# Kernel optimization log

Hardware: AMD Instinct MI355X
Metric: run time of the kernel (lower is better)

Reference implementation:

```python
import jax, jax.numpy as jnp
import numpy as np

N, E, B, H, L = 50000, 500000, 64, 64, 4


def setup_inputs() -> dict:
    key = jax.random.key(0)
    ks = jax.random.split(key, 32)
    def w(k, shp, fan_in):
        s = 1.0 / np.sqrt(fan_in)
        return jax.random.uniform(k, shp, jnp.float32, -s, s)
    inp = {
        "v0": jax.random.normal(ks[0], (N, 1), jnp.float32),
        "v1": jax.random.normal(ks[1], (N, 1), jnp.float32),
        "dist": jax.random.uniform(ks[2], (E, 1), jnp.float32),
        "edge_index": jax.random.randint(ks[3], (2, E), 0, N, jnp.int32),
        "batch": jnp.sort(jax.random.randint(ks[4], (N,), 0, B, jnp.int32)),
        "batch_size": B,
        # embeddings / per-input linears
        "wte": jax.random.normal(ks[5], (2, H), jnp.float32),
        "W_in0": w(ks[6], (H, 1), 1), "b_in0": w(ks[7], (H,), 1),
        "W_in1": w(ks[8], (H, 1), 1), "b_in1": w(ks[9], (H,), 1),
        "W_out0": w(ks[10], (1, H), H), "b_out0": w(ks[11], (1,), H),
        "W_out1": w(ks[12], (1, H), H), "b_out1": w(ks[13], (1,), H),
        "W_edge": w(ks[14], (H, 1), 1), "b_edge": w(ks[15], (H,), 1),
        # shared GraphBlock (ModuleList([block]*L) shares weights)
        "W_el": w(ks[16], (H, 2 * H), 2 * H), "b_el": w(ks[17], (H,), 2 * H),
        "W_n1": w(ks[18], (4 * H, 3 * H), 3 * H), "b_n1": w(ks[19], (4 * H,), 3 * H),
        "W_n2": w(ks[20], (H, 4 * H), 4 * H), "b_n2": w(ks[21], (H,), 4 * H),
        "W_gl": w(ks[22], (H, 2 * H), 2 * H), "b_gl": w(ks[23], (H,), 2 * H),
        # shared LSTMCell
        "W_ih": w(ks[24], (4 * H, H), H), "W_hh": w(ks[25], (4 * H, H), H),
        "b_ih": w(ks[26], (4 * H,), H), "b_hh": w(ks[27], (4 * H,), H),
    }
    return inp


def _forward(v0, v1, dist, edge_index, batch, batch_size,
             wte, W_in0, b_in0, W_in1, b_in1, W_out0, b_out0, W_out1, b_out1,
             W_edge, b_edge, W_el, b_el, W_n1, b_n1, W_n2, b_n2, W_gl, b_gl,
             W_ih, W_hh, b_ih, b_hh):
    # x = sum_i (type_embedding_i + Linear_i(v_i))  -> [N, H]
    x = (wte[0] + v0 @ W_in0.T + b_in0) + (wte[1] + v1 @ W_in1.T + b_in1)
    e = dist @ W_edge.T + b_edge                      # [E, H]
    u = jnp.zeros((batch_size, x.shape[-1]), x.dtype)  # [B, H]
    row, col = edge_index[0], edge_index[1]
    n_nodes = x.shape[0]
    cs = []
    for _ in range(L):  # shared weights across layers (faithful to [block]*L)
        # edge MLP on gathered source features, scatter-max to destination nodes
        msg = jax.nn.relu(jnp.concatenate([x[row], e], axis=-1) @ W_el.T + b_el)
        agg = jax.ops.segment_max(msg, col, num_segments=n_nodes)
        agg = jnp.where(jnp.isfinite(agg), agg, 0.0)  # empty segments -> 0
        # node MLP with residual
        h1 = jax.nn.relu(jnp.concatenate([agg, x, u[batch]], axis=-1) @ W_n1.T + b_n1)
        x = x + h1 @ W_n2.T + b_n2
        # global update: per-graph max over nodes
        x_u = jax.ops.segment_max(x, batch, num_segments=batch_size)
        x_u = jnp.where(jnp.isfinite(x_u), x_u, 0.0)
        u = u + jax.nn.relu(jnp.concatenate([x_u, u], axis=-1) @ W_gl.T + b_gl)
        # LSTMCell with zero initial (h, c) every layer (hidden_states=None path)
        gates = u @ W_ih.T + b_ih + b_hh  # h_prev = 0 so W_hh term vanishes
        i_g, f_g, g_g, o_g = jnp.split(gates, 4, axis=-1)
        c = jax.nn.sigmoid(i_g) * jnp.tanh(g_g)        # c_prev = 0
        u = jax.nn.sigmoid(o_g) * jnp.tanh(c)
        cs.append(c)
    outs = jnp.stack([x @ W_out0.T + b_out0, x @ W_out1.T + b_out1])  # [2, N, 1]
    return outs, jnp.stack(cs)  # ([2,N,1], [L,B,H])


def reference(v0, v1, dist, edge_index, batch, batch_size,
              wte, W_in0, b_in0, W_in1, b_in1, W_out0, b_out0, W_out1, b_out1,
              W_edge, b_edge, W_el, b_el, W_n1, b_n1, W_n2, b_n2, W_gl, b_gl,
              W_ih, W_hh, b_ih, b_hh):
    return _forward(v0, v1, dist, edge_index, batch, batch_size,
                    wte, W_in0, b_in0, W_in1, b_in1, W_out0, b_out0, W_out1, b_out1,
                    W_edge, b_edge, W_el, b_el, W_n1, b_n1, W_n2, b_n2, W_gl, b_gl,
                    W_ih, W_hh, b_ih, b_hh)
```

## Files before the change

### kernel.cpp

```cpp
#include <hip/hip_runtime.h>


typedef __attribute__((ext_vector_type(8))) short short8;
typedef __attribute__((ext_vector_type(4))) float f32x4;

__device__ __forceinline__ unsigned short f2bf(float f) {
  union { float f; unsigned u; } v; v.f = f;
  unsigned r = v.u + 0x7FFFu + ((v.u >> 16) & 1u);
  return (unsigned short)(r >> 16);
}
__device__ __forceinline__ float bf2f(unsigned short s) {
  return __uint_as_float((unsigned)s << 16);
}
__device__ __forceinline__ unsigned enc_ordered(float f) {
  unsigned u = __float_as_uint(f);
  return (u >> 31) ? ~u : (u | 0x80000000u);
}

__global__ void k_init(const float* __restrict__ v0, const float* __restrict__ v1,
                       const float* __restrict__ wte,
                       const float* __restrict__ Wi0, const float* __restrict__ bi0,
                       const float* __restrict__ Wi1, const float* __restrict__ bi1,
                       const int* __restrict__ batch,
                       int* __restrict__ gstart, int* __restrict__ gend,
                       float* __restrict__ x,
                       float* __restrict__ u, unsigned* __restrict__ xu_enc,
                       unsigned short* __restrict__ W1b, unsigned short* __restrict__ W2b,
                       unsigned short* __restrict__ Welb,
                       const float* __restrict__ W_n1, const float* __restrict__ W_n2,
                       const float* __restrict__ W_el,
                       const float* __restrict__ b_el,
                       const float* __restrict__ W_edge, const float* __restrict__ b_edge,
                       float* __restrict__ p, float* __restrict__ q,
                       float* __restrict__ c0, float* __restrict__ c1,
                       float* __restrict__ c2,
                       int* __restrict__ deg, int* __restrict__ cur, int N) {
  int gt = blockIdx.x * 256 + threadIdx.x;
  int NH = N * 64;
  if (gt < NH) {
    int n = gt >> 6, h = gt & 63;
    x[gt] = wte[h] + wte[64 + h] + bi0[h] + bi1[h] + v0[n] * Wi0[h] + v1[n] * Wi1[h];
    if (h == 0) {
      int bg = batch[n];
      if (n == 0 || batch[n - 1] != bg) gstart[bg] = n;
      if (n == N - 1 || batch[n + 1] != bg) gend[bg] = n + 1;
    }
    return;
  }
  int i = gt - NH;
  if (i < 4096) {
    u[i] = 0.f;
  } else if (i < 8192) {
    xu_enc[i - 4096] = 0x007FFFFFu;
  } else if (i < 8192 + 49152) {
    int j = i - 8192;
    W1b[j] = f2bf(W_n1[j]);
  } else if (i < 8192 + 49152 + 16384) {
    int j = i - 57344;
    W2b[j] = f2bf(W_n2[j]);
  } else if (i < 77824) {
    int j = i - 73728;
    Welb[j] = f2bf(W_el[(j >> 6) * 128 + (j & 63)]);
  } else if (i < 77824 + N) {
    deg[i - 77824] = 0;
  } else if (i < 77824 + 2 * N) {
    cur[i - 77824 - N] = 0;
  } else if (i < 77824 + 2 * N + 64) {
    int h = i - 77824 - 2 * N;
    float pp = 0.f, qq = 0.f, s0 = 0.f, s1 = 0.f, s2 = 0.f;
    for (int k = 0; k < 64; ++k) {
      float w2 = W_el[h * 128 + 64 + k];
      pp += w2 * W_edge[k];
      qq += w2 * b_edge[k];
      float w1 = W_el[h * 128 + k];
      float base = wte[k] + wte[64 + k] + bi0[k] + bi1[k];
      s0 += w1 * base;
      s1 += w1 * Wi0[k];
      s2 += w1 * Wi1[k];
    }
    p[h] = pp; q[h] = qq + b_el[h];
    c0[h] = s0; c1[h] = s1; c2[h] = s2;
  }
}

__global__ __launch_bounds__(256) void k_hist(const int* __restrict__ eidx,
                                              int* __restrict__ deg, int E) {
  int e = blockIdx.x * 256 + threadIdx.x;
  if (e < E) atomicAdd(&deg[eidx[E + e]], 1);
}

__global__ __launch_bounds__(256) void k_scan1(const int* __restrict__ deg,
                                               int* __restrict__ off,
                                               int* __restrict__ bsum, int N) {
  __shared__ int s[256];
  int b = blockIdx.x, t = threadIdx.x;
  int i0 = b * 512 + t * 2;
  int v0 = (i0 < N) ? deg[i0] : 0;
  int v1 = (i0 + 1 < N) ? deg[i0 + 1] : 0;
  int sum = v0 + v1;
  s[t] = sum;
  __syncthreads();
  for (int d = 1; d < 256; d <<= 1) {
    int val = (t >= d) ? s[t - d] : 0;
    __syncthreads();
    s[t] += val;
    __syncthreads();
  }
  int excl = s[t] - sum;
  if (i0 < N) off[i0] = excl + v0;
  if (i0 + 1 < N) off[i0 + 1] = excl + v0 + v1;
  if (t == 255) bsum[b] = s[t];
}

__global__ void k_scan2(int* __restrict__ bsum, int nb) {
  __shared__ int s[128];
  int t = threadIdx.x;
  int v = (t < nb) ? bsum[t] : 0;
  s[t] = v;
  __syncthreads();
  for (int d = 1; d < 128; d <<= 1) {
    int val = (t >= d) ? s[t - d] : 0;
    __syncthreads();
    s[t] += val;
    __syncthreads();
  }
  if (t < nb) bsum[t] = s[t] - v;
}

__global__ __launch_bounds__(256) void k_scatter(const int* __restrict__ eidx,
                                                 const float* __restrict__ dist,
                                                 const int* __restrict__ off,
                                                 const int* __restrict__ bsum,
                                                 int* __restrict__ cur,
                                                 uint2* __restrict__ spack, int E) {
  int e = blockIdx.x * 256 + threadIdx.x;
  if (e >= E) return;
  int c = eidx[E + e];
  int base = (c == 0) ? 0 : (off[c - 1] + bsum[(c - 1) >> 9]);
  int pos = base + atomicAdd(&cur[c], 1);
  spack[pos] = make_uint2((unsigned)eidx[e] | ((unsigned)(c & 31) << 27),
                          __float_as_uint(dist[e]));
}

template <int MODE>
__global__ __launch_bounds__(256) void k_node(
    const int* __restrict__ off, const int* __restrict__ bsum,
    const uint2* __restrict__ spack,
    const float* __restrict__ p, const float* __restrict__ q,
    const float* __restrict__ c0, const float* __restrict__ c1,
    const float* __restrict__ c2,
    const float* __restrict__ v0, const float* __restrict__ v1,
    float* __restrict__ x, unsigned short* __restrict__ y_bf,
    const int* __restrict__ batch, const float* __restrict__ u,
    const unsigned short* __restrict__ W1b, const unsigned short* __restrict__ W2b,
    const unsigned short* __restrict__ Welb,
    const float* __restrict__ b_n1, const float* __restrict__ b_n2,
    unsigned* __restrict__ xu_enc,
    float* __restrict__ bmaxA, float* __restrict__ bmaxB,
    int* __restrict__ bgidA, int* __restrict__ bgidB,
    const float* __restrict__ Wo0, const float* __restrict__ bo0,
    const float* __restrict__ Wo1, const float* __restrict__ bo1,
    float* __restrict__ outp, int N) {
  __shared__ __align__(16) char inb[32 * 384];
  __shared__ __align__(16) char h1T[32 * 512];
  __shared__ uint2 smeta[256];
  __shared__ int sgb[32];
  int t = threadIdx.x;
  int n0 = blockIdx.x * 32;
  int lane = t & 63, wv = t >> 6;
  int lr = lane & 15;
  int lk8 = (lane >> 4) << 3;
  int jo = (lane >> 4) << 2;
  int swzr = (lr & 7) << 4;
  int h0 = wv * 16 + jo;

  float4 xo[2];
#pragma unroll
  for (int nt = 0; nt < 2; ++nt) {
    int node = n0 + nt * 16 + lr;
    xo[nt] = (node < N) ? *(const float4*)(x + (size_t)node * 64 + h0)
                        : make_float4(0.f, 0.f, 0.f, 0.f);
  }
  int nd_s = t >> 3, ko = t & 7;
  int node_s = n0 + nd_s;
  float4 ua = make_float4(0.f, 0.f, 0.f, 0.f), ub = ua;
  if (node_s < N) {
    int g = batch[node_s];
    const float4* u4 = (const float4*)u;
    ua = u4[g * 16 + ko * 2];
    ub = u4[g * 16 + ko * 2 + 1];
  }
  if (t < 32) sgb[t] = batch[min(n0 + t, N - 1)];

  int* aggi = (int*)h1T;
#pragma unroll
  for (int i = 0; i < 8; ++i) aggi[t + i * 256] = 0;

#pragma unroll
  for (int nt = 0; nt < 2; ++nt) {
    int nd = nt * 16 + lr;
    unsigned lo = (unsigned)f2bf(xo[nt].x) | ((unsigned)f2bf(xo[nt].y) << 16);
    unsigned hi = (unsigned)f2bf(xo[nt].z) | ((unsigned)f2bf(xo[nt].w) << 16);
    *(uint2*)(inb + nd * 384 + ((128 + h0 * 2) ^ ((nd & 7) << 4))) = make_uint2(lo, hi);
  }
  {
    int swz = (nd_s & 7) << 4;
    uint4 uv;
    uv.x = f2bf(ua.x) | ((unsigned)f2bf(ua.y) << 16);
    uv.y = f2bf(ua.z) | ((unsigned)f2bf(ua.w) << 16);
    uv.z = f2bf(ub.x) | ((unsigned)f2bf(ub.y) << 16);
    uv.w = f2bf(ub.z) | ((unsigned)f2bf(ub.w) << 16);
    *(uint4*)(inb + nd_s * 384 + ((256 + ko * 16) ^ swz)) = uv;
  }
  __syncthreads();

  {
    int last = min(n0 + 31, N - 1);
    int ebase = (n0 == 0) ? 0 : (off[n0 - 1] + bsum[(n0 - 1) >> 9]);
    int eend = off[last] + bsum[last >> 9];
    int total = eend - ebase;
    int q4 = total >> 2;
    int wb = ebase + wv * q4;
    int we = (wv == 3) ? eend : (wb + q4);
    uint2* sm = smeta + wv * 64;
    int half = lane >> 5, l31 = lane & 31;
    const unsigned* y32 = (const unsigned*)y_bf + l31;
    float2 p2 = *(const float2*)(p + 2 * l31);
    float2 q2 = *(const float2*)(q + 2 * l31);
    float2 c02 = make_float2(0.f, 0.f), c12 = c02, c22 = c02;
    if (MODE == 0) {
      c02 = *(const float2*)(c0 + 2 * l31);
      c12 = *(const float2*)(c1 + 2 * l31);
      c22 = *(const float2*)(c2 + 2 * l31);
    }
    float m0 = 0.f, m1 = 0.f;
    int ccur = -1;
    uint2 r = make_uint2(0u, 0u);
    if (wb < we) {
      int cnt = min(64, we - wb);
      if (lane < cnt) r = spack[wb + lane];
    }
    for (int cb = wb; cb < we; cb += 64) {
      int ccnt = min(64, we - cb);
      sm[lane] = r;
      int nb = cb + 64;
      if (nb < we) {
        int ncnt = we - nb;
        if (lane < ncnt) r = spack[nb + lane];
      }
      int nfull = ccnt >> 1;
      int i = 0;
      for (; i + 8 <= nfull; i += 8) {
        uint2 e[8]; unsigned yd[8]; float va[8], vb[8];
#pragma unroll
        for (int k = 0; k < 8; ++k) e[k] = sm[2 * (i + k) + half];
#pragma unroll
        for (int k = 0; k < 8; ++k) {
          unsigned row = e[k].x & 0x07FFFFFFu;
          if (MODE == 0) { va[k] = v0[row]; vb[k] = v1[row]; }
          else yd[k] = y32[row << 5];
        }
#pragma unroll
        for (int k = 0; k < 8; ++k) {
          float y0f, y1f;
          if (MODE == 0) {
            y0f = fmaf(vb[k], c22.x, fmaf(va[k], c12.x, c02.x));
            y1f = fmaf(vb[k], c22.y, fmaf(va[k], c12.y, c02.y));
          } else {
            y0f = __uint_as_float(yd[k] << 16);
            y1f = __uint_as_float(yd[k] & 0xFFFF0000u);
          }
          float d = __uint_as_float(e[k].y);
          float g0 = fmaxf(fmaf(d, p2.x, y0f + q2.x), 0.f);
          float g1 = fmaxf(fmaf(d, p2.y, y1f + q2.y), 0.f);
          int c = (int)(e[k].x >> 27);
          if (c != ccur) {
            if (ccur >= 0) {
              atomicMax(&aggi[ccur * 64 + 2 * l31], __float_as_int(m0));
              atomicMax(&aggi[ccur * 64 + 2 * l31 + 1], __float_as_int(m1));
            }
            ccur = c; m0 = g0; m1 = g1;
          } else { m0 = fmaxf(m0, g0); m1 = fmaxf(m1, g1); }
        }
      }
      for (; 2 * i < ccnt; ++i) {
        int idx = 2 * i + half;
        bool val = idx < ccnt;
        uint2 e = sm[val ? idx : 0];
        unsigned row = e.x & 0x07FFFFFFu;
        float y0f, y1f;
        if (MODE == 0) {
          float a = v0[row], b = v1[row];
          y0f = fmaf(b, c22.x, fmaf(a, c12.x, c02.x));
          y1f = fmaf(b, c22.y, fmaf(a, c12.y, c02.y));
        } else {
          unsigned yd = y32[row << 5];
          y0f = __uint_as_float(yd << 16);
          y1f = __uint_as_float(yd & 0xFFFF0000u);
        }
        float d = __uint_as_float(e.y);
        float g0 = val ? fmaxf(fmaf(d, p2.x, y0f + q2.x), 0.f) : 0.f;
        float g1 = val ? fmaxf(fmaf(d, p2.y, y1f + q2.y), 0.f) : 0.f;
        int c = val ? (int)(e.x >> 27) : ccur;
        if (c != ccur) {
          if (ccur >= 0) {
            atomicMax(&aggi[ccur * 64 + 2 * l31], __float_as_int(m0));
            atomicMax(&aggi[ccur * 64 + 2 * l31 + 1], __float_as_int(m1));
          }
          ccur = c; m0 = g0; m1 = g1;
        } else { m0 = fmaxf(m0, g0); m1 = fmaxf(m1, g1); }
      }
    }
    if (ccur >= 0) {
      atomicMax(&aggi[ccur * 64 + 2 * l31], __float_as_int(m0));
      atomicMax(&aggi[ccur * 64 + 2 * l31 + 1], __float_as_int(m1));
    }
  }
  __syncthreads();

  {
    int swz = (nd_s & 7) << 4;
    const float4* ag4 = (const float4*)(h1T);
    float4 aa = ag4[nd_s * 16 + ko * 2];
    float4 ab = ag4[nd_s * 16 + ko * 2 + 1];
    uint4 av;
    av.x = f2bf(aa.x) | ((unsigned)f2bf(aa.y) << 16);
    av.y = f2bf(aa.z) | ((unsigned)f2bf(aa.w) << 16);
    av.z = f2bf(ab.x) | ((unsigned)f2bf(ab.y) << 16);
    av.w = f2bf(ab.z) | ((unsigned)f2bf(ab.w) << 16);
    *(uint4*)(inb + nd_s * 384 + ((ko * 16) ^ swz)) = av;
  }
  __syncthreads();

  int w = wv;

  f32x4 acc[4][2];
#pragma unroll
  for (int ot = 0; ot < 4; ++ot)
#pragma unroll
    for (int nt = 0; nt < 2; ++nt) acc[ot][nt] = (f32x4){0.f, 0.f, 0.f, 0.f};
  const unsigned short* W1p = W1b + (w * 64 + lr) * 192 + lk8;
#pragma unroll
  for (int ks = 0; ks < 6; ++ks) {
    int kb = ks * 64 + lk8 * 2;
    short8 b0 = *(const short8*)(inb + lr * 384 + (kb ^ swzr));
    short8 b1 = *(const short8*)(inb + (16 + lr) * 384 + (kb ^ swzr));
#pragma unroll
    for (int ot = 0; ot < 4; ++ot) {
      short8 a = *(const short8*)(W1p + ot * (16 * 192) + ks * 32);
      acc[ot][0] = __builtin_amdgcn_mfma_f32_16x16x32_bf16(a, b0, acc[ot][0], 0, 0, 0);
      acc[ot][1] = __builtin_amdgcn_mfma_f32_16x16x32_bf16(a, b1, acc[ot][1], 0, 0, 0);
    }
  }
  __syncthreads();
#pragma unroll
  for (int ot = 0; ot < 4; ++ot) {
    int o = w * 64 + ot * 16 + jo;
    float4 bs = *(const float4*)(b_n1 + o);
#pragma unroll
    for (int nt = 0; nt < 2; ++nt) {
      int nd = nt * 16 + lr;
      unsigned lo = (unsigned)f2bf(fmaxf(acc[ot][nt][0] + bs.x, 0.f)) |
                    ((unsigned)f2bf(fmaxf(acc[ot][nt][1] + bs.y, 0.f)) << 16);
      unsigned hi = (unsigned)f2bf(fmaxf(acc[ot][nt][2] + bs.z, 0.f)) |
                    ((unsigned)f2bf(fmaxf(acc[ot][nt][3] + bs.w, 0.f)) << 16);
      *(uint2*)(h1T + nd * 512 + ((o * 2) ^ ((nd & 7) << 4))) = make_uint2(lo, hi);
    }
  }
  __syncthreads();

  f32x4 acc2[2] = {{0.f, 0.f, 0.f, 0.f}, {0.f, 0.f, 0.f, 0.f}};
  const unsigned short* W2p = W2b + (w * 16 + lr) * 256 + lk8;
#pragma unroll
  for (int ks = 0; ks < 8; ++ks) {
    short8 a = *(const short8*)(W2p + ks * 32);
    int kb = ks * 64 + lk8 * 2;
    short8 b0 = *(const short8*)(h1T + lr * 512 + (kb ^ swzr));
    short8 b1 = *(const short8*)(h1T + (16 + lr) * 512 + (kb ^ swzr));
    acc2[0] = __builtin_amdgcn_mfma_f32_16x16x32_bf16(a, b0, acc2[0], 0, 0, 0);
    acc2[1] = __builtin_amdgcn_mfma_f32_16x16x32_bf16(a, b1, acc2[1], 0, 0, 0);
  }
  float4 b2 = *(const float4*)(b_n2 + h0);
  char* xnb = inb;
  float4 xn[2];
#pragma unroll
  for (int nt = 0; nt < 2; ++nt) {
    int nd = nt * 16 + lr;
    int node = n0 + nd;
    xn[nt].x = xo[nt].x + acc2[nt][0] + b2.x;
    xn[nt].y = xo[nt].y + acc2[nt][1] + b2.y;
    xn[nt].z = xo[nt].z + acc2[nt][2] + b2.z;
    xn[nt].w = xo[nt].w + acc2[nt][3] + b2.w;
    if (node >= N) xn[nt] = make_float4(0.f, 0.f, 0.f, 0.f);
    if (MODE != 2 && node < N) *(float4*)(x + (size_t)node * 64 + h0) = xn[nt];
    if (MODE != 2) {
      unsigned lo = (unsigned)f2bf(xn[nt].x) | ((unsigned)f2bf(xn[nt].y) << 16);
      unsigned hi = (unsigned)f2bf(xn[nt].z) | ((unsigned)f2bf(xn[nt].w) << 16);
      *(uint2*)(xnb + nd * 128 + ((h0 * 2) ^ ((nd & 7) << 4))) = make_uint2(lo, hi);
    }
  }

  {
    const float NEG = -__builtin_huge_valf();
    int gA = sgb[0], gB = sgb[31];
    float a0 = NEG, a1 = NEG, a2 = NEG, a3 = NEG;
    float e0 = NEG, e1 = NEG, e2 = NEG, e3 = NEG;
#pragma unroll
    for (int nt = 0; nt < 2; ++nt) {
      int nd = nt * 16 + lr;
      if (n0 + nd < N) {
        int g = sgb[nd];
        if (g == gA) {
          a0 = fmaxf(a0, xn[nt].x); a1 = fmaxf(a1, xn[nt].y);
          a2 = fmaxf(a2, xn[nt].z); a3 = fmaxf(a3, xn[nt].w);
        } else if (g == gB) {
          e0 = fmaxf(e0, xn[nt].x); e1 = fmaxf(e1, xn[nt].y);
          e2 = fmaxf(e2, xn[nt].z); e3 = fmaxf(e3, xn[nt].w);
        } else {
          unsigned* xe = xu_enc + g * 64 + h0;
          atomicMax(xe + 0, enc_ordered(xn[nt].x));
          atomicMax(xe + 1, enc_ordered(xn[nt].y));
          atomicMax(xe + 2, enc_ordered(xn[nt].z));
          atomicMax(xe + 3, enc_ordered(xn[nt].w));
        }
      }
    }
#pragma unroll
    for (int msk = 1; msk <= 8; msk <<= 1) {
      a0 = fmaxf(a0, __shfl_xor(a0, msk)); a1 = fmaxf(a1, __shfl_xor(a1, msk));
      a2 = fmaxf(a2, __shfl_xor(a2, msk)); a3 = fmaxf(a3, __shfl_xor(a3, msk));
      e0 = fmaxf(e0, __shfl_xor(e0, msk)); e1 = fmaxf(e1, __shfl_xor(e1, msk));
      e2 = fmaxf(e2, __shfl_xor(e2, msk)); e3 = fmaxf(e3, __shfl_xor(e3, msk));
    }
    if (lr == 0) {
      size_t base = (size_t)blockIdx.x * 64 + h0;
      bmaxA[base + 0] = a0; bmaxA[base + 1] = a1;
      bmaxA[base + 2] = a2; bmaxA[base + 3] = a3;
      bmaxB[base + 0] = e0; bmaxB[base + 1] = e1;
      bmaxB[base + 2] = e2; bmaxB[base + 3] = e3;
    }
    if (t == 0) {
      bgidA[blockIdx.x] = gA;
      bgidB[blockIdx.x] = (gB == gA) ? -1 : gB;
    }
  }
  __syncthreads();

  if (MODE != 2) {
    f32x4 acc3[2] = {{0.f, 0.f, 0.f, 0.f}, {0.f, 0.f, 0.f, 0.f}};
    const unsigned short* W3p = Welb + (w * 16 + lr) * 64 + lk8;
#pragma unroll
    for (int ks = 0; ks < 2; ++ks) {
      short8 a = *(const short8*)(W3p + ks * 32);
      int kb = ks * 64 + lk8 * 2;
      short8 b0 = *(const short8*)(xnb + lr * 128 + (kb ^ swzr));
      short8 b1 = *(const short8*)(xnb + (16 + lr) * 128 + (kb ^ swzr));
      acc3[0] = __builtin_amdgcn_mfma_f32_16x16x32_bf16(a, b0, acc3[0], 0, 0, 0);
      acc3[1] = __builtin_amdgcn_mfma_f32_16x16x32_bf16(a, b1, acc3[1], 0, 0, 0);
    }
    int o0 = w * 16 + jo;
#pragma unroll
    for (int nt = 0; nt < 2; ++nt) {
      int node = n0 + nt * 16 + lr;
      if (node < N) {
        unsigned lo = (unsigned)f2bf(acc3[nt][0]) | ((unsigned)f2bf(acc3[nt][1]) << 16);
        unsigned hi = (unsigned)f2bf(acc3[nt][2]) | ((unsigned)f2bf(acc3[nt][3]) << 16);
        *(uint2*)(y_bf + (size_t)node * 64 + o0) = make_uint2(lo, hi);
      }
    }
  } else {
    float4 w0 = *(const float4*)(Wo0 + h0);
    float4 w1 = *(const float4*)(Wo1 + h0);
    float* ow = (float*)h1T;
#pragma unroll
    for (int nt = 0; nt < 2; ++nt) {
      float p0 = xn[nt].x * w0.x + xn[nt].y * w0.y + xn[nt].z * w0.z + xn[nt].w * w0.w;
      float p1 = xn[nt].x * w1.x + xn[nt].y * w1.y + xn[nt].z * w1.z + xn[nt].w * w1.w;
      p0 += __shfl_xor(p0, 16); p0 += __shfl_xor(p0, 32);
      p1 += __shfl_xor(p1, 16); p1 += __shfl_xor(p1, 32);
      if (lane < 16) {
        ow[w * 64 + 0 + nt * 16 + lr] = p0;
        ow[w * 64 + 32 + nt * 16 + lr] = p1;
      }
    }
    __syncthreads();
    if (t < 64) {
      int oi = t >> 5, nd = t & 31;
      int node = n0 + nd;
      if (node < N) {
        float v = ow[0 * 64 + oi * 32 + nd] + ow[1 * 64 + oi * 32 + nd] +
                  ow[2 * 64 + oi * 32 + nd] + ow[3 * 64 + oi * 32 + nd];
        v += (oi ? bo1[0] : bo0[0]);
        outp[(size_t)oi * N + node] = v;
      }
    }
  }
}

__global__ __launch_bounds__(256) void k_graph(const int* __restrict__ gstart,
                                               const int* __restrict__ gend,
                                               const float* __restrict__ bmaxA,
                                               const float* __restrict__ bmaxB,
                                               const int* __restrict__ bgidA,
                                               const int* __restrict__ bgidB,
                                               unsigned* __restrict__ xu_enc,
                                               float* __restrict__ u,
                                               const float* __restrict__ W_gl,
                                               const float* __restrict__ b_gl,
                                               const float* __restrict__ W_ih,
                                               const float* __restrict__ b_ih,
                                               const float* __restrict__ b_hh,
                                               float* __restrict__ c_out) {
  __shared__ float red[4][3][64];
  __shared__ float xu_s[64], us[64], un[64];
  int g = blockIdx.x;
  int t = threadIdx.x, h = t & 63, qd = t >> 6;
  const float NEG = -__builtin_huge_valf();

  float m = NEG;
  int gs = gstart[g], ge = gend[g];
  if (gs < ge) {
    int bs = gs >> 5, be = (ge - 1) >> 5;
    for (int b = bs + qd; b <= be; b += 4) {
      if (bgidA[b] == g) m = fmaxf(m, bmaxA[(size_t)b * 64 + h]);
      if (bgidB[b] == g) m = fmaxf(m, bmaxB[(size_t)b * 64 + h]);
    }
  }
  red[qd][0][h] = m;
  __syncthreads();
  if (qd == 0) {
    m = fmaxf(fmaxf(red[0][0][h], red[1][0][h]), fmaxf(red[2][0][h], red[3][0][h]));
    unsigned Ev = xu_enc[g * 64 + h];
    float fd = (Ev & 0x80000000u) ? __uint_as_float(Ev & 0x7FFFFFFFu)
                                  : __uint_as_float(~Ev);
    m = fmaxf(m, fd);
    xu_enc[g * 64 + h] = 0x007FFFFFu;
    xu_s[h] = isfinite(m) ? m : 0.f;
    us[h] = u[g * 64 + h];
  }
  __syncthreads();

  float pre = 0.f;
  {
    const float* Wrow = W_gl + h * 128 + qd * 32;
    const float* src = (qd < 2) ? (xu_s + qd * 32) : (us + (qd - 2) * 32);
#pragma unroll 8
    for (int k = 0; k < 32; ++k) pre += src[k] * Wrow[k];
  }
  red[qd][0][h] = pre;
  __syncthreads();
  if (qd == 0) {
    float prs = red[0][0][h] + red[1][0][h] + red[2][0][h] + red[3][0][h] + b_gl[h];
    un[h] = us[h] + fmaxf(prs, 0.f);
  }
  __syncthreads();

  float gi = 0.f, gg = 0.f, go = 0.f;
#pragma unroll 4
  for (int k = qd * 16; k < qd * 16 + 16; ++k) {
    float uv = un[k];
    gi += uv * W_ih[h * 64 + k];
    gg += uv * W_ih[(128 + h) * 64 + k];
    go += uv * W_ih[(192 + h) * 64 + k];
  }
  red[qd][0][h] = gi; red[qd][1][h] = gg; red[qd][2][h] = go;
  __syncthreads();
  if (qd == 0) {
    gi = red[0][0][h] + red[1][0][h] + red[2][0][h] + red[3][0][h] + b_ih[h] + b_hh[h];
    gg = red[0][1][h] + red[1][1][h] + red[2][1][h] + red[3][1][h] +
         b_ih[128 + h] + b_hh[128 + h];
    go = red[0][2][h] + red[1][2][h] + red[2][2][h] + red[3][2][h] +
         b_ih[192 + h] + b_hh[192 + h];
    float cc = (1.f / (1.f + expf(-gi))) * tanhf(gg);
    float u2v = (1.f / (1.f + expf(-go))) * tanhf(cc);
    c_out[g * 64 + h] = cc;
    u[g * 64 + h] = u2v;
  }
}

extern "C" void kernel_launch(void* const* d_in, const int* in_sizes, int n_in,
                              void* d_out, int out_size, void* d_ws, size_t ws_size,
                              hipStream_t stream) {
  const float* v0 = (const float*)d_in[0];
  const float* v1 = (const float*)d_in[1];
  const float* dist = (const float*)d_in[2];
  const int* eidx = (const int*)d_in[3];
  const int* batch = (const int*)d_in[4];
  const float* wte = (const float*)d_in[6];
  const float* Wi0 = (const float*)d_in[7];
  const float* bi0 = (const float*)d_in[8];
  const float* Wi1 = (const float*)d_in[9];
  const float* bi1 = (const float*)d_in[10];
  const float* Wo0 = (const float*)d_in[11];
  const float* bo0 = (const float*)d_in[12];
  const float* Wo1 = (const float*)d_in[13];
  const float* bo1 = (const float*)d_in[14];
  const float* W_edge = (const float*)d_in[15];
  const float* b_edge = (const float*)d_in[16];
  const float* W_el = (const float*)d_in[17];
  const float* b_el = (const float*)d_in[18];
  const float* W_n1 = (const float*)d_in[19];
  const float* b_n1 = (const float*)d_in[20];
  const float* W_n2 = (const float*)d_in[21];
  const float* b_n2 = (const float*)d_in[22];
  const float* W_gl = (const float*)d_in[23];
  const float* b_gl = (const float*)d_in[24];
  const float* W_ih = (const float*)d_in[25];
  const float* b_ih = (const float*)d_in[27];
  const float* b_hh = (const float*)d_in[28];

  const int N = in_sizes[0];
  const int E = in_sizes[2];
  const int NH = N * 64;
  const int NB512 = (N + 511) / 512;
  const int nblk = (N + 31) / 32;

  float* ws = (float*)d_ws;
  float* x = ws;
  float* u = x + NH;
  unsigned* xu_enc = (unsigned*)(u + 4096);
  float* p = (float*)(xu_enc + 4096);
  float* q = p + 64;
  float* c0 = q + 64;
  float* c1 = c0 + 64;
  float* c2 = c1 + 64;
  unsigned short* W1b = (unsigned short*)(c2 + 64);
  unsigned short* W2b = W1b + 49152;
  unsigned short* Welb = W2b + 16384;
  unsigned short* y_bf = Welb + 4096;
  int* deg = (int*)(y_bf + NH);
  int* off = deg + N;
  int* cur = off + N;
  int* bsum = cur + N;
  int* gstart = bsum + 128;
  int* gend = gstart + 64;
  int* bgidA = gend + 64;
  int* bgidB = bgidA + nblk;
  float* bmaxA = (float*)(bgidB + nblk);
  float* bmaxB = bmaxA + (size_t)nblk * 64;
  uint2* spack = (uint2*)(((size_t)(bmaxB + (size_t)nblk * 64) + 15) & ~(size_t)15);

  float* outp = (float*)d_out;

  k_init<<<(NH + 77824 + 2 * N + 64 + 255) / 256, 256, 0, stream>>>(
      v0, v1, wte, Wi0, bi0, Wi1, bi1, batch, gstart, gend, x,
      u, xu_enc, W1b, W2b, Welb, W_n1, W_n2, W_el, b_el, W_edge, b_edge,
      p, q, c0, c1, c2, deg, cur, N);
  k_hist<<<(E + 255) / 256, 256, 0, stream>>>(eidx, deg, E);
  k_scan1<<<NB512, 256, 0, stream>>>(deg, off, bsum, N);
  k_scan2<<<1, 128, 0, stream>>>(bsum, NB512);
  k_scatter<<<(E + 255) / 256, 256, 0, stream>>>(eidx, dist, off, bsum, cur, spack, E);

  for (int l = 0; l < 4; ++l) {
    if (l == 0) {
      k_node<0><<<nblk, 256, 0, stream>>>(off, bsum, spack, p, q, c0, c1, c2, v0, v1,
                                          x, y_bf, batch, u, W1b, W2b, Welb, b_n1, b_n2,
                                          xu_enc, bmaxA, bmaxB, bgidA, bgidB,
                                          Wo0, bo0, Wo1, bo1, outp, N);
    } else if (l < 3) {
      k_node<1><<<nblk, 256, 0, stream>>>(off, bsum, spack, p, q, c0, c1, c2, v0, v1,
                                          x, y_bf, batch, u, W1b, W2b, Welb, b_n1, b_n2,
                                          xu_enc, bmaxA, bmaxB, bgidA, bgidB,
                                          Wo0, bo0, Wo1, bo1, outp, N);
    } else {
      k_node<2><<<nblk, 256, 0, stream>>>(off, bsum, spack, p, q, c0, c1, c2, v0, v1,
                                          x, y_bf, batch, u, W1b, W2b, Welb, b_n1, b_n2,
                                          xu_enc, bmaxA, bmaxB, bgidA, bgidB,
                                          Wo0, bo0, Wo1, bo1, outp, N);
    }
    k_graph<<<64, 256, 0, stream>>>(gstart, gend, bmaxA, bmaxB, bgidA, bgidB,
                                    xu_enc, u, W_gl, b_gl, W_ih, b_ih, b_hh,
                                    outp + 2 * N + l * 4096);
  }
}
```

Measured before the change: 313.9 us.

## Halve node tile to 16 per block and compute initial x inline in layer 0

The node kernel now handles 16 nodes per block instead of 32. It uses half the shared memory and accumulator registers and launches twice as many blocks, which should raise occupancy and spread edge work across more workgroups. The initial x embedding is no longer materialised in k_init; layer 0 computes it on the fly from v0 and v1, which saves a full N×64 write and read. In exchange, weight tiles are reloaded per 16 nodes, so weight traffic and per-block overhead grow, and the col-bit tag in spack shrinks to 4 bits to match the smaller tile.

New measurement: 409.5 us. +30.5%, slower.

```diff
diff --git a/kernel.cpp b/kernel.cpp
--- a/kernel.cpp
+++ b/kernel.cpp
@@ -23,7 +23,6 @@
                        const float* __restrict__ Wi1, const float* __restrict__ bi1,
                        const int* __restrict__ batch,
                        int* __restrict__ gstart, int* __restrict__ gend,
-                       float* __restrict__ x,
                        float* __restrict__ u, unsigned* __restrict__ xu_enc,
                        unsigned short* __restrict__ W1b, unsigned short* __restrict__ W2b,
                        unsigned short* __restrict__ Welb,
@@ -35,19 +34,7 @@
                        float* __restrict__ c0, float* __restrict__ c1,
                        float* __restrict__ c2,
                        int* __restrict__ deg, int* __restrict__ cur, int N) {
-  int gt = blockIdx.x * 256 + threadIdx.x;
-  int NH = N * 64;
-  if (gt < NH) {
-    int n = gt >> 6, h = gt & 63;
-    x[gt] = wte[h] + wte[64 + h] + bi0[h] + bi1[h] + v0[n] * Wi0[h] + v1[n] * Wi1[h];
-    if (h == 0) {
-      int bg = batch[n];
-      if (n == 0 || batch[n - 1] != bg) gstart[bg] = n;
-      if (n == N - 1 || batch[n + 1] != bg) gend[bg] = n + 1;
-    }
-    return;
-  }
-  int i = gt - NH;
+  int i = blockIdx.x * 256 + threadIdx.x;
   if (i < 4096) {
     u[i] = 0.f;
   } else if (i < 8192) {
@@ -65,8 +52,13 @@
     deg[i - 77824] = 0;
   } else if (i < 77824 + 2 * N) {
     cur[i - 77824 - N] = 0;
-  } else if (i < 77824 + 2 * N + 64) {
-    int h = i - 77824 - 2 * N;
+  } else if (i < 77824 + 3 * N) {
+    int n = i - 77824 - 2 * N;
+    int bg = batch[n];
+    if (n == 0 || batch[n - 1] != bg) gstart[bg] = n;
+    if (n == N - 1 || batch[n + 1] != bg) gend[bg] = n + 1;
+  } else if (i < 77824 + 3 * N + 64) {
+    int h = i - 77824 - 3 * N;
     float pp = 0.f, qq = 0.f, s0 = 0.f, s1 = 0.f, s2 = 0.f;
     for (int k = 0; k < 64; ++k) {
       float w2 = W_el[h * 128 + 64 + k];
@@ -138,7 +130,7 @@
   int c = eidx[E + e];
   int base = (c == 0) ? 0 : (off[c - 1] + bsum[(c - 1) >> 9]);
   int pos = base + atomicAdd(&cur[c], 1);
-  spack[pos] = make_uint2((unsigned)eidx[e] | ((unsigned)(c & 31) << 27),
+  spack[pos] = make_uint2((unsigned)eidx[e] | ((unsigned)(c & 15) << 27),
                           __float_as_uint(dist[e]));
 }
 
@@ -150,6 +142,9 @@
     const float* __restrict__ c0, const float* __restrict__ c1,
     const float* __restrict__ c2,
     const float* __restrict__ v0, const float* __restrict__ v1,
+    const float* __restrict__ wte,
+    const float* __restrict__ Wi0, const float* __restrict__ bi0,
+    const float* __restrict__ Wi1, const float* __restrict__ bi1,
     float* __restrict__ x, unsigned short* __restrict__ y_bf,
     const int* __restrict__ batch, const float* __restrict__ u,
     const unsigned short* __restrict__ W1b, const unsigned short* __restrict__ W2b,
@@ -161,12 +156,12 @@
     const float* __restrict__ Wo0, const float* __restrict__ bo0,
     const float* __restrict__ Wo1, const float* __restrict__ bo1,
     float* __restrict__ outp, int N) {
-  __shared__ __align__(16) char inb[32 * 384];
-  __shared__ __align__(16) char h1T[32 * 512];
+  __shared__ __align__(16) char inb[16 * 384];
+  __shared__ __align__(16) char h1T[16 * 512];
   __shared__ uint2 smeta[256];
-  __shared__ int sgb[32];
+  __shared__ int sgb[16];
   int t = threadIdx.x;
-  int n0 = blockIdx.x * 32;
+  int n0 = blockIdx.x * 16;
   int lane = t & 63, wv = t >> 6;
   int lr = lane & 15;
   int lk8 = (lane >> 4) << 3;
@@ -174,36 +169,51 @@
   int swzr = (lr & 7) << 4;
   int h0 = wv * 16 + jo;
 
-  float4 xo[2];
-#pragma unroll
-  for (int nt = 0; nt < 2; ++nt) {
-    int node = n0 + nt * 16 + lr;
-    xo[nt] = (node < N) ? *(const float4*)(x + (size_t)node * 64 + h0)
-                        : make_float4(0.f, 0.f, 0.f, 0.f);
+  float4 xo;
+  {
+    int node = n0 + lr;
+    if (MODE == 0) {
+      float4 wA = *(const float4*)(wte + h0);
+      float4 wB = *(const float4*)(wte + 64 + h0);
+      float4 bA = *(const float4*)(bi0 + h0);
+      float4 bB = *(const float4*)(bi1 + h0);
+      float4 w0v = *(const float4*)(Wi0 + h0);
+      float4 w1v = *(const float4*)(Wi1 + h0);
+      float a = (node < N) ? v0[node] : 0.f;
+      float b = (node < N) ? v1[node] : 0.f;
+      xo.x = wA.x + wB.x + bA.x + bB.x + a * w0v.x + b * w1v.x;
+      xo.y = wA.y + wB.y + bA.y + bB.y + a * w0v.y + b * w1v.y;
+      xo.z = wA.z + wB.z + bA.z + bB.z + a * w0v.z + b * w1v.z;
+      xo.w = wA.w + wB.w + bA.w + bB.w + a * w0v.w + b * w1v.w;
+    } else {
+      xo = (node < N) ? *(const float4*)(x + (size_t)node * 64 + h0)
+                      : make_float4(0.f, 0.f, 0.f, 0.f);
+    }
   }
   int nd_s = t >> 3, ko = t & 7;
-  int node_s = n0 + nd_s;
   float4 ua = make_float4(0.f, 0.f, 0.f, 0.f), ub = ua;
-  if (node_s < N) {
-    int g = batch[node_s];
-    const float4* u4 = (const float4*)u;
-    ua = u4[g * 16 + ko * 2];
-    ub = u4[g * 16 + ko * 2 + 1];
-  }
-  if (t < 32) sgb[t] = batch[min(n0 + t, N - 1)];
+  if (t < 128) {
+    int node_s = n0 + nd_s;
+    if (node_s < N) {
+      int g = batch[node_s];
+      const float4* u4 = (const float4*)u;
+      ua = u4[g * 16 + ko * 2];
+      ub = u4[g * 16 + ko * 2 + 1];
+    }
+  }
+  if (t < 16) sgb[t] = batch[min(n0 + t, N - 1)];
 
   int* aggi = (int*)h1T;
 #pragma unroll
-  for (int i = 0; i < 8; ++i) aggi[t + i * 256] = 0;
-
-#pragma unroll
-  for (int nt = 0; nt < 2; ++nt) {
-    int nd = nt * 16 + lr;
-    unsigned lo = (unsigned)f2bf(xo[nt].x) | ((unsigned)f2bf(xo[nt].y) << 16);
-    unsigned hi = (unsigned)f2bf(xo[nt].z) | ((unsigned)f2bf(xo[nt].w) << 16);
+  for (int i = 0; i < 4; ++i) aggi[t + i * 256] = 0;
+
+  {
+    int nd = lr;
+    unsigned lo = (unsigned)f2bf(xo.x) | ((unsigned)f2bf(xo.y) << 16);
+    unsigned hi = (unsigned)f2bf(xo.z) | ((unsigned)f2bf(xo.w) << 16);
     *(uint2*)(inb + nd * 384 + ((128 + h0 * 2) ^ ((nd & 7) << 4))) = make_uint2(lo, hi);
   }
-  {
+  if (t < 128) {
     int swz = (nd_s & 7) << 4;
     uint4 uv;
     uv.x = f2bf(ua.x) | ((unsigned)f2bf(ua.y) << 16);
@@ -215,7 +225,7 @@
   __syncthreads();
 
   {
-    int last = min(n0 + 31, N - 1);
+    int last = min(n0 + 15, N - 1);
     int ebase = (n0 == 0) ? 0 : (off[n0 - 1] + bsum[(n0 - 1) >> 9]);
     int eend = off[last] + bsum[last >> 9];
     int total = eend - ebase;
@@ -318,7 +328,7 @@
   }
   __syncthreads();
 
-  {
+  if (t < 128) {
     int swz = (nd_s & 7) << 4;
     const float4* ag4 = (const float4*)(h1T);
     float4 aa = ag4[nd_s * 16 + ko * 2];
@@ -334,22 +344,18 @@
 
   int w = wv;
 
-  f32x4 acc[4][2];
-#pragma unroll
-  for (int ot = 0; ot < 4; ++ot)
-#pragma unroll
-    for (int nt = 0; nt < 2; ++nt) acc[ot][nt] = (f32x4){0.f, 0.f, 0.f, 0.f};
+  f32x4 acc[4];
+#pragma unroll
+  for (int ot = 0; ot < 4; ++ot) acc[ot] = (f32x4){0.f, 0.f, 0.f, 0.f};
   const unsigned short* W1p = W1b + (w * 64 + lr) * 192 + lk8;
 #pragma unroll
   for (int ks = 0; ks < 6; ++ks) {
     int kb = ks * 64 + lk8 * 2;
     short8 b0 = *(const short8*)(inb + lr * 384 + (kb ^ swzr));
-    short8 b1 = *(const short8*)(inb + (16 + lr) * 384 + (kb ^ swzr));
 #pragma unroll
     for (int ot = 0; ot < 4; ++ot) {
       short8 a = *(const short8*)(W1p + ot * (16 * 192) + ks * 32);
-      acc[ot][0] = __builtin_amdgcn_mfma_f32_16x16x32_bf16(a, b0, acc[ot][0], 0, 0, 0);
-      acc[ot][1] = __builtin_amdgcn_mfma_f32_16x16x32_bf16(a, b1, acc[ot][1], 0, 0, 0);
+      acc[ot] = __builtin_amdgcn_mfma_f32_16x16x32_bf16(a, b0, acc[ot], 0, 0, 0);
     }
   }
   __syncthreads();
@@ -357,71 +363,62 @@
   for (int ot = 0; ot < 4; ++ot) {
     int o = w * 64 + ot * 16 + jo;
     float4 bs = *(const float4*)(b_n1 + o);
-#pragma unroll
-    for (int nt = 0; nt < 2; ++nt) {
-      int nd = nt * 16 + lr;
-      unsigned lo = (unsigned)f2bf(fmaxf(acc[ot][nt][0] + bs.x, 0.f)) |
-                    ((unsigned)f2bf(fmaxf(acc[ot][nt][1] + bs.y, 0.f)) << 16);
-      unsigned hi = (unsigned)f2bf(fmaxf(acc[ot][nt][2] + bs.z, 0.f)) |
-                    ((unsigned)f2bf(fmaxf(acc[ot][nt][3] + bs.w, 0.f)) << 16);
-      *(uint2*)(h1T + nd * 512 + ((o * 2) ^ ((nd & 7) << 4))) = make_uint2(lo, hi);
-    }
-  }
-  __syncthreads();
-
-  f32x4 acc2[2] = {{0.f, 0.f, 0.f, 0.f}, {0.f, 0.f, 0.f, 0.f}};
+    int nd = lr;
+    unsigned lo = (unsigned)f2bf(fmaxf(acc[ot][0] + bs.x, 0.f)) |
+                  ((unsigned)f2bf(fmaxf(acc[ot][1] + bs.y, 0.f)) << 16);
+    unsigned hi = (unsigned)f2bf(fmaxf(acc[ot][2] + bs.z, 0.f)) |
+                  ((unsigned)f2bf(fmaxf(acc[ot][3] + bs.w, 0.f)) << 16);
+    *(uint2*)(h1T + nd * 512 + ((o * 2) ^ ((nd & 7) << 4))) = make_uint2(lo, hi);
+  }
+  __syncthreads();
+
+  f32x4 acc2 = (f32x4){0.f, 0.f, 0.f, 0.f};
   const unsigned short* W2p = W2b + (w * 16 + lr) * 256 + lk8;
 #pragma unroll
   for (int ks = 0; ks < 8; ++ks) {
     short8 a = *(const short8*)(W2p + ks * 32);
     int kb = ks * 64 + lk8 * 2;
     short8 b0 = *(const short8*)(h1T + lr * 512 + (kb ^ swzr));
-    short8 b1 = *(const short8*)(h1T + (16 + lr) * 512 + (kb ^ swzr));
-    acc2[0] = __builtin_amdgcn_mfma_f32_16x16x32_bf16(a, b0, acc2[0], 0, 0, 0);
-    acc2[1] = __builtin_amdgcn_mfma_f32_16x16x32_bf16(a, b1, acc2[1], 0, 0, 0);
+    acc2 = __builtin_amdgcn_mfma_f32_16x16x32_bf16(a, b0, acc2, 0, 0, 0);
   }
   float4 b2 = *(const float4*)(b_n2 + h0);
   char* xnb = inb;
-  float4 xn[2];
-#pragma unroll
-  for (int nt = 0; nt < 2; ++nt) {
-    int nd = nt * 16 + lr;
+  float4 xn;
+  {
+    int nd = lr;
     int node = n0 + nd;
-    xn[nt].x = xo[nt].x + acc2[nt][0] + b2.x;
-    xn[nt].y = xo[nt].y + acc2[nt][1] + b2.y;
-    xn[nt].z = xo[nt].z + acc2[nt][2] + b2.z;
-    xn[nt].w = xo[nt].w + acc2[nt][3] + b2.w;
-    if (node >= N) xn[nt] = make_float4(0.f, 0.f, 0.f, 0.f);
-    if (MODE != 2 && node < N) *(float4*)(x + (size_t)node * 64 + h0) = xn[nt];
+    xn.x = xo.x + acc2[0] + b2.x;
+    xn.y = xo.y + acc2[1] + b2.y;
+    xn.z = xo.z + acc2[2] + b2.z;
+    xn.w = xo.w + acc2[3] + b2.w;
+    if (node >= N) xn = make_float4(0.f, 0.f, 0.f, 0.f);
+    if (MODE != 2 && node < N) *(float4*)(x + (size_t)node * 64 + h0) = xn;
     if (MODE != 2) {
-      unsigned lo = (unsigned)f2bf(xn[nt].x) | ((unsigned)f2bf(xn[nt].y) << 16);
-      unsigned hi = (unsigned)f2bf(xn[nt].z) | ((unsigned)f2bf(xn[nt].w) << 16);
+      unsigned lo = (unsigned)f2bf(xn.x) | ((unsigned)f2bf(xn.y) << 16);
+      unsigned hi = (unsigned)f2bf(xn.z) | ((unsigned)f2bf(xn.w) << 16);
       *(uint2*)(xnb + nd * 128 + ((h0 * 2) ^ ((nd & 7) << 4))) = make_uint2(lo, hi);
     }
   }
 
   {
     const float NEG = -__builtin_huge_valf();
-    int gA = sgb[0], gB = sgb[31];
+    int gA = sgb[0], gB = sgb[15];
     float a0 = NEG, a1 = NEG, a2 = NEG, a3 = NEG;
     float e0 = NEG, e1 = NEG, e2 = NEG, e3 = NEG;
-#pragma unroll
-    for (int nt = 0; nt < 2; ++nt) {
-      int nd = nt * 16 + lr;
+    {
+      int nd = lr;
       if (n0 + nd < N) {
         int g = sgb[nd];
         if (g == gA) {
-          a0 = fmaxf(a0, xn[nt].x); a1 = fmaxf(a1, xn[nt].y);
-          a2 = fmaxf(a2, xn[nt].z); a3 = fmaxf(a3, xn[nt].w);
+          a0 = xn.x; a1 = xn.y; a2 = xn.z; a3 = xn.w;
         } else if (g == gB) {
-          e0 = fmaxf(e0, xn[nt].x); e1 = fmaxf(e1, xn[nt].y);
-          e2 = fmaxf(e2, xn[nt].z); e3 = fmaxf(e3, xn[nt].w);
+          e0 = xn.x; e1 = xn.y; e2 = xn.z; e3 = xn.w;
         } else {
           unsigned* xe = xu_enc + g * 64 + h0;
-          atomicMax(xe + 0, enc_ordered(xn[nt].x));
-          atomicMax(xe + 1, enc_ordered(xn[nt].y));
-          atomicMax(xe + 2, enc_ordered(xn[nt].z));
-          atomicMax(xe + 3, enc_ordered(xn[nt].w));
+          atomicMax(xe + 0, enc_ordered(xn.x));
+          atomicMax(xe + 1, enc_ordered(xn.y));
+          atomicMax(xe + 2, enc_ordered(xn.z));
+          atomicMax(xe + 3, enc_ordered(xn.w));
         }
       }
     }
@@ -447,49 +444,43 @@
   __syncthreads();
 
   if (MODE != 2) {
-    f32x4 acc3[2] = {{0.f, 0.f, 0.f, 0.f}, {0.f, 0.f, 0.f, 0.f}};
+    f32x4 acc3 = (f32x4){0.f, 0.f, 0.f, 0.f};
     const unsigned short* W3p = Welb + (w * 16 + lr) * 64 + lk8;
 #pragma unroll
     for (int ks = 0; ks < 2; ++ks) {
       short8 a = *(const short8*)(W3p + ks * 32);
       int kb = ks * 64 + lk8 * 2;
       short8 b0 = *(const short8*)(xnb + lr * 128 + (kb ^ swzr));
-      short8 b1 = *(const short8*)(xnb + (16 + lr) * 128 + (kb ^ swzr));
-      acc3[0] = __builtin_amdgcn_mfma_f32_16x16x32_bf16(a, b0, acc3[0], 0, 0, 0);
-      acc3[1] = __builtin_amdgcn_mfma_f32_16x16x32_bf16(a, b1, acc3[1], 0, 0, 0);
+      acc3 = __builtin_amdgcn_mfma_f32_16x16x32_bf16(a, b0, acc3, 0, 0, 0);
     }
     int o0 = w * 16 + jo;
-#pragma unroll
-    for (int nt = 0; nt < 2; ++nt) {
-      int node = n0 + nt * 16 + lr;
-      if (node < N) {
-        unsigned lo = (unsigned)f2bf(acc3[nt][0]) | ((unsigned)f2bf(acc3[nt][1]) << 16);
-        unsigned hi = (unsigned)f2bf(acc3[nt][2]) | ((unsigned)f2bf(acc3[nt][3]) << 16);
-        *(uint2*)(y_bf + (size_t)node * 64 + o0) = make_uint2(lo, hi);
-      }
+    int node = n0 + lr;
+    if (node < N) {
+      unsigned lo = (unsigned)f2bf(acc3[0]) | ((unsigned)f2bf(acc3[1]) << 16);
+      unsigned hi = (unsigned)f2bf(acc3[2]) | ((unsigned)f2bf(acc3[3]) << 16);
+      *(uint2*)(y_bf + (size_t)node * 64 + o0) = make_uint2(lo, hi);
     }
   } else {
     float4 w0 = *(const float4*)(Wo0 + h0);
     float4 w1 = *(const float4*)(Wo1 + h0);
     float* ow = (float*)h1T;
-#pragma unroll
-    for (int nt = 0; nt < 2; ++nt) {
-      float p0 = xn[nt].x * w0.x + xn[nt].y * w0.y + xn[nt].z * w0.z + xn[nt].w * w0.w;
-      float p1 = xn[nt].x * w1.x + xn[nt].y * w1.y + xn[nt].z * w1.z + xn[nt].w * w1.w;
+    {
+      float p0 = xn.x * w0.x + xn.y * w0.y + xn.z * w0.z + xn.w * w0.w;
+      float p1 = xn.x * w1.x + xn.y * w1.y + xn.z * w1.z + xn.w * w1.w;
       p0 += __shfl_xor(p0, 16); p0 += __shfl_xor(p0, 32);
       p1 += __shfl_xor(p1, 16); p1 += __shfl_xor(p1, 32);
       if (lane < 16) {
-        ow[w * 64 + 0 + nt * 16 + lr] = p0;
-        ow[w * 64 + 32 + nt * 16 + lr] = p1;
+        ow[w * 32 + 0 + lr] = p0;
+        ow[w * 32 + 16 + lr] = p1;
       }
     }
     __syncthreads();
-    if (t < 64) {
-      int oi = t >> 5, nd = t & 31;
+    if (t < 32) {
+      int oi = t >> 4, nd = t & 15;
       int node = n0 + nd;
       if (node < N) {
-        float v = ow[0 * 64 + oi * 32 + nd] + ow[1 * 64 + oi * 32 + nd] +
-                  ow[2 * 64 + oi * 32 + nd] + ow[3 * 64 + oi * 32 + nd];
+        float v = ow[0 * 32 + oi * 16 + nd] + ow[1 * 32 + oi * 16 + nd] +
+                  ow[2 * 32 + oi * 16 + nd] + ow[3 * 32 + oi * 16 + nd];
         v += (oi ? bo1[0] : bo0[0]);
         outp[(size_t)oi * N + node] = v;
       }
@@ -520,7 +511,7 @@
   float m = NEG;
   int gs = gstart[g], ge = gend[g];
   if (gs < ge) {
-    int bs = gs >> 5, be = (ge - 1) >> 5;
+    int bs = gs >> 4, be = (ge - 1) >> 4;
     for (int b = bs + qd; b <= be; b += 4) {
       if (bgidA[b] == g) m = fmaxf(m, bmaxA[(size_t)b * 64 + h]);
       if (bgidB[b] == g) m = fmaxf(m, bmaxB[(size_t)b * 64 + h]);
@@ -613,7 +604,7 @@
   const int E = in_sizes[2];
   const int NH = N * 64;
   const int NB512 = (N + 511) / 512;
-  const int nblk = (N + 31) / 32;
+  const int nblk = (N + 15) / 16;
 
   float* ws = (float*)d_ws;
   float* x = ws;
@@ -642,8 +633,8 @@
 
   float* outp = (float*)d_out;
 
-  k_init<<<(NH + 77824 + 2 * N + 64 + 255) / 256, 256, 0, stream>>>(
-      v0, v1, wte, Wi0, bi0, Wi1, bi1, batch, gstart, gend, x,
+  k_init<<<(77824 + 3 * N + 64 + 255) / 256, 256, 0, stream>>>(
+      v0, v1, wte, Wi0, bi0, Wi1, bi1, batch, gstart, gend,
       u, xu_enc, W1b, W2b, Welb, W_n1, W_n2, W_el, b_el, W_edge, b_edge,
       p, q, c0, c1, c2, deg, cur, N);
   k_hist<<<(E + 255) / 256, 256, 0, stream>>>(eidx, deg, E);
@@ -654,16 +645,19 @@
   for (int l = 0; l < 4; ++l) {
     if (l == 0) {
       k_node<0><<<nblk, 256, 0, stream>>>(off, bsum, spack, p, q, c0, c1, c2, v0, v1,
+                                          wte, Wi0, bi0, Wi1, bi1,
                                           x, y_bf, batch, u, W1b, W2b, Welb, b_n1, b_n2,
                                           xu_enc, bmaxA, bmaxB, bgidA, bgidB,
                                           Wo0, bo0, Wo1, bo1, outp, N);
     } else if (l < 3) {
       k_node<1><<<nblk, 256, 0, stream>>>(off, bsum, spack, p, q, c0, c1, c2, v0, v1,
+                                          wte, Wi0, bi0, Wi1, bi1,
                                           x, y_bf, batch, u, W1b, W2b, Welb, b_n1, b_n2,
                                           xu_enc, bmaxA, bmaxB, bgidA, bgidB,
                                           Wo0, bo0, Wo1, bo1, outp, N);
     } else {
       k_node<2><<<nblk, 256, 0, stream>>>(off, bsum, spack, p, q, c0, c1, c2, v0, v1,
+                                          wte, Wi0, bi0, Wi1, bi1,
                                           x, y_bf, batch, u, W1b, W2b, Welb, b_n1, b_n2,
                                           xu_enc, bmaxA, bmaxB, bgidA, bgidB,
                                           Wo0, bo0, Wo1, bo1, outp, N);
```
